# Kernel optimization log

Hardware: AMD Instinct MI355X
Metric: run time of the kernel (lower is better)

The kernel has to match this reference:

```python
import jax, jax.numpy as jnp
import numpy as np

B, S, D = 8, 2048, 256
H = 2
DK = D // H
DH = 1024  # conv hidden
K = 9
PAD = (K - 1) // 2
EPS = 1e-5


def _layernorm(x, g, b):
    mu = jnp.mean(x, axis=-1, keepdims=True)
    var = jnp.mean(jnp.square(x - mu), axis=-1, keepdims=True)
    return (x - mu) * jax.lax.rsqrt(var + EPS) * g + b


def setup_inputs() -> dict:
    key = jax.random.key(0)
    ks = jax.random.split(key, 12)
    sc = 0.02
    batch = jax.random.normal(ks[0], (B, S, D), dtype=jnp.float32)
    # padding mask: True = past end of sequence
    lengths = jax.random.randint(ks[1], (B,), S // 2, S + 1)
    mask = jnp.arange(S)[None, :] >= lengths[:, None]
    return {
        "batch": batch,
        "mask": mask,
        "wq": jax.random.normal(ks[2], (D, D), jnp.float32) * sc,
        "bq": jnp.zeros((D,), jnp.float32),
        "wk": jax.random.normal(ks[3], (D, D), jnp.float32) * sc,
        "bk": jnp.zeros((D,), jnp.float32),
        "wv": jax.random.normal(ks[4], (D, D), jnp.float32) * sc,
        "bv": jnp.zeros((D,), jnp.float32),
        "wo": jax.random.normal(ks[5], (D, D), jnp.float32) * sc,
        "bo": jnp.zeros((D,), jnp.float32),
        "ln1_g": jnp.ones((D,), jnp.float32),
        "ln1_b": jnp.zeros((D,), jnp.float32),
        "conv1_w": jax.random.normal(ks[6], (DH, D, K), jnp.float32) * sc,
        "conv1_b": jnp.zeros((DH,), jnp.float32),
        "conv2_w": jax.random.normal(ks[7], (D, DH, 1), jnp.float32) * sc,
        "conv2_b": jnp.zeros((D,), jnp.float32),
        "ln2_g": jnp.ones((D,), jnp.float32),
        "ln2_b": jnp.zeros((D,), jnp.float32),
    }


def reference(batch, mask, wq, bq, wk, bk, wv, bv, wo, bo, ln1_g, ln1_b,
              conv1_w, conv1_b, conv2_w, conv2_b, ln2_g, ln2_b):
    b, s, d = batch.shape
    # --- multi-head self-attention ---
    q = (batch @ wq.T + bq).reshape(b, s, H, DK)
    k = (batch @ wk.T + bk).reshape(b, s, H, DK)
    v = (batch @ wv.T + bv).reshape(b, s, H, DK)
    scores = jnp.einsum('bqhd,bkhd->bhqk', q, k) / np.sqrt(d).astype(np.float32)
    scores = jnp.where(mask[:, None, None, :], -jnp.inf, scores)
    attn = jax.nn.softmax(scores, axis=-1)
    ctx = jnp.einsum('bhqk,bkhd->bqhd', attn, v).reshape(b, s, d)
    seq = _layernorm(batch + ctx @ wo.T + bo, ln1_g, ln1_b)
    seq = jnp.where(mask[..., None], 0.0, seq)
    # --- conv FFN ---
    h = jax.lax.conv_general_dilated(
        seq.transpose(0, 2, 1), conv1_w, window_strides=(1,),
        padding=[(PAD, PAD)], dimension_numbers=('NCH', 'OIH', 'NCH'))
    h = jax.nn.relu(h + conv1_b[None, :, None])
    out = jnp.einsum('bhs,oh->bos', h, conv2_w[:, :, 0]) + conv2_b[None, :, None]
    seq = _layernorm(seq + out.transpose(0, 2, 1), ln2_g, ln2_b)
    return jnp.where(mask[..., None], 0.0, seq)
```

## Files before the change

kernel.cpp:

```cpp
#include <hip/hip_runtime.h>

typedef unsigned char  u8;
typedef unsigned short u16;
typedef unsigned int   u32;
typedef __attribute__((ext_vector_type(4))) float f32x4;
typedef __attribute__((ext_vector_type(8))) __bf16 bf16x8;
typedef __attribute__((ext_vector_type(4))) u32  u32x4;
typedef __attribute__((ext_vector_type(2))) u32  u32x2;

__device__ __forceinline__ float bf2f(u16 h){ u32 u = ((u32)h)<<16; return __builtin_bit_cast(float, u); }
__device__ __forceinline__ u16  f2bf(float f){
  u32 u = __builtin_bit_cast(u32, f);
  u32 r = u + 0x7FFFu + ((u>>16)&1u);
  return (u16)(r>>16);
}

typedef const __attribute__((address_space(1))) u32 gas_u32;
typedef __attribute__((address_space(3))) u32 las_u32;
__device__ __forceinline__ void gll16(const void* g, void* l){
  __builtin_amdgcn_global_load_lds((gas_u32*)g, (las_u32*)l, 16, 0, 0);
}

__device__ __forceinline__ f32x4 mfma16(bf16x8 a, bf16x8 b, f32x4 c){
  return __builtin_amdgcn_mfma_f32_16x16x32_bf16(a, b, c, 0, 0, 0);
}

__device__ __forceinline__ bf16x8 ldsr8(const u16* p){
  u32x4 v = *(const u32x4*)p;
  return __builtin_bit_cast(bf16x8, v);
}

__device__ __forceinline__ void xcd_remap(int &m_idx, int &n_idx){
  const int Mt = gridDim.x;
  const int fid = blockIdx.x + Mt*blockIdx.y;
  const int xcd = fid & 7, k = fid >> 3;
  const int mpx = Mt >> 3;
  m_idx = xcd*mpx + (k % mpx);
  n_idx = k / mpx;
}

__global__ __launch_bounds__(256)
void prep_big(const float* __restrict__ batch,
              const float* __restrict__ wq, const float* __restrict__ wk,
              const float* __restrict__ wv, const float* __restrict__ wo,
              const float* __restrict__ w2, const float* __restrict__ w1,
              u16* __restrict__ batchc, u16* __restrict__ wqc, u16* __restrict__ w1r)
{
  const int bid = blockIdx.x, tid = threadIdx.x;
  if (bid < 4096){
    const int i = bid*1024 + tid*4;
    f32x4 v = *(const f32x4*)&batch[i];
    u32x2 o;
    o[0] = (u32)f2bf(v[0]) | ((u32)f2bf(v[1])<<16);
    o[1] = (u32)f2bf(v[2]) | ((u32)f2bf(v[3])<<16);
    *(u32x2*)&batchc[i] = o;
  } else if (bid < 4608){
    const int i = (bid-4096)*1024 + tid*4;
    const float* s; int off;
    if      (i < 65536)  { s = wq; off = i; }
    else if (i < 131072) { s = wk; off = i - 65536; }
    else if (i < 196608) { s = wv; off = i - 131072; }
    else if (i < 262144) { s = wo; off = i - 196608; }
    else                 { s = w2; off = i - 262144; }
    f32x4 v = *(const f32x4*)&s[off];
    u32x2 o;
    o[0] = (u32)f2bf(v[0]) | ((u32)f2bf(v[1])<<16);
    o[1] = (u32)f2bf(v[2]) | ((u32)f2bf(v[3])<<16);
    *(u32x2*)&wqc[i] = o;
  } else {
    const int idx = (bid-4608)*256 + tid;
    const int c = idx / 2304;
    const int t = idx - c*2304;
    const int i = t / 9;
    const int kk = t - i*9;
    w1r[c*2304 + kk*256 + i] = f2bf(w1[idx]);
  }
}

__global__ __launch_bounds__(256)
void prep_small(const float* p0,const float* p1,const float* p2,const float* p3,
                const float* p4,const float* p5,const float* p6,const float* p7,
                const float* p8,const float* p9,
                u16* __restrict__ params, const void* __restrict__ mraw,
                u16* __restrict__ cmask, u32* __restrict__ lengths)
{
  const int bid = blockIdx.x, tid = threadIdx.x;
  if (bid == 0){
    const float* ps[10] = {p0,p1,p2,p3,p4,p5,p6,p7,p8,p9};
    const int  off[10] = {0,256,512,768,1024,1280,1536,1792,2048,3072};
    const int  len[10] = {256,256,256,256,256,256,256,256,1024,256};
    for (int a=0;a<10;++a)
      for (int i=tid;i<len[a];i+=256)
        params[off[a]+i] = f2bf(ps[a][i]);
  } else {
    const u8*  pb8  = (const u8*)mraw;
    const u16* pb16 = (const u16*)mraw;
    const u32* pb32 = (const u32*)mraw;
    __shared__ int bad8, bad16, nz8, nz16;
    __shared__ int slen[8];
    if (tid==0){ bad8=0; bad16=0; nz8=0; nz16=0; }
    if (tid<8) slen[tid] = 2048;
    __syncthreads();
    for (int i=tid;i<16384;i+=256){
      u8 v = pb8[i]; int row = i & 2047;
      if (v>1) atomicOr(&bad8,1);
      if (v){ atomicOr(&nz8,1); if (row<1024) atomicOr(&bad8,1); }
      if (row>0 && pb8[i-1]==1 && v==0) atomicOr(&bad8,1);
    }
    for (int i=tid;i<8192;i+=256){
      u16 v = pb16[i]; int row = i & 2047;
      if (!(v==0 || v==0x3F80)) atomicOr(&bad16,1);
      if (v){ atomicOr(&nz16,1); if (row<1024) atomicOr(&bad16,1); }
      if (row>0 && pb16[i-1]==0x3F80 && v==0) atomicOr(&bad16,1);
    }
    __syncthreads();
    const int mode = (!bad8 && nz8) ? 1 : ((!bad16 && nz16) ? 2 : 0);
    for (int i=tid;i<16384;i+=256){
      u16 m;
      if (mode==1)      m = pb8[i]  ? 1 : 0;
      else if (mode==2) m = pb16[i] ? 1 : 0;
      else              m = pb32[i] ? 1 : 0;
      cmask[i] = m;
      if (m) atomicMin(&slen[i>>11], i&2047);
    }
    __syncthreads();
    if (tid<8) lengths[tid] = (u32)slen[tid];
  }
}

__global__ __launch_bounds__(256)
void zero_halo(u16* __restrict__ seq1p)
{
  const int idx = blockIdx.x*256 + threadIdx.x;
  const int b = idx>>11, t = idx&2047;
  const int r = t>>8, c = t&255;
  const int row = (r<4) ? r : (2052 + r - 4);
  seq1p[((size_t)b*2056 + row)*256 + c] = 0;
}

__global__ __launch_bounds__(256)
void gemm_qkv(const u16* __restrict__ A, const u16* __restrict__ W,
              const u16* __restrict__ bias, u16* __restrict__ qbase,
              const u16* __restrict__ cmask)
{
  __shared__ __align__(16) u16 aL[2][4096];
  __shared__ __align__(16) u16 bL[2][4096];
  const int tid = threadIdx.x, lane = tid&63, w = tid>>6;
  const int wm = w>>1, wn = w&1, lr = lane&15, lg = lane>>4;
  int mi, ni; xcd_remap(mi, ni);
  const int m0 = mi*128, n0 = ni*128;
  if (cmask[m0] != 0) return;

  f32x4 acc[4][4];
#pragma unroll
  for (int i=0;i<4;++i)
#pragma unroll
    for (int j=0;j<4;++j) acc[i][j] = f32x4{0.f,0.f,0.f,0.f};

  auto stage = [&](int buf, int kk){
#pragma unroll
    for (int i=0;i<2;++i){
      const int chunk = w*2+i;
      const int boff  = chunk*1024 + lane*16;
      const int r = boff>>6;
      const int cb = (boff&63) ^ (((r>>1)&3)<<4);
      const int c = cb>>1;
      gll16(&A[(size_t)(m0+r)*256 + kk*32 + c], &aL[buf][chunk*512]);
      gll16(&W[(size_t)(n0+r)*256 + kk*32 + c], &bL[buf][chunk*512]);
    }
  };

  stage(0,0);
  __syncthreads();
  for (int kk=0; kk<8; ++kk){
    if (kk+1<8) stage((kk+1)&1, kk+1);
    const u16* ab = aL[kk&1];
    const u16* bb = bL[kk&1];
    bf16x8 af[4], bv[4];
#pragma unroll
    for (int m=0;m<4;++m){
      const int ra = wm*64+m*16+lr;
      af[m] = ldsr8(&ab[(ra*64 + ((lg*16) ^ (((ra>>1)&3)<<4)))>>1]);
    }
#pragma unroll
    for (int n=0;n<4;++n){
      const int rb = wn*64+n*16+lr;
      bv[n] = ldsr8(&bb[(rb*64 + ((lg*16) ^ (((rb>>1)&3)<<4)))>>1]);
    }
#pragma unroll
    for (int m=0;m<4;++m)
#pragma unroll
      for (int n=0;n<4;++n)
        acc[m][n] = mfma16(af[m], bv[n], acc[m][n]);
    __syncthreads();
  }
#pragma unroll
  for (int m=0;m<4;++m)
#pragma unroll
    for (int n=0;n<4;++n)
#pragma unroll
      for (int r=0;r<4;++r){
        const int row = m0 + wm*64 + m*16 + lg*4 + r;
        const int col = n0 + wn*64 + n*16 + lr;
        const int which = col>>8, ch = col&255;
        float v = acc[m][n][r] + bf2f(bias[col]);
        qbase[(size_t)which*4194304 + (size_t)row*256 + ch] = f2bf(v);
      }
}

__global__ __launch_bounds__(256, 4)
void conv1_gemm(const u16* __restrict__ Ap, const u16* __restrict__ W1r,
                const u16* __restrict__ b1, u16* __restrict__ Hout,
                const u16* __restrict__ cmask)
{
  __shared__ __align__(16) u16 aL[2][4096];
  __shared__ __align__(16) u16 bL[2][4096];
  const int tid = threadIdx.x, lane = tid&63, w = tid>>6;
  const int wm = w>>1, wn = w&1, lr = lane&15, lg = lane>>4;
  int mi, ni; xcd_remap(mi, ni);
  const int m0 = mi*128, n0 = ni*128;
  if (cmask[m0] != 0) return;
  const int b = m0>>11, s0 = m0&2047;
  const size_t abase = ((size_t)b*2056 + s0)*256;

  f32x4 acc[4][4];
#pragma unroll
  for (int i=0;i<4;++i)
#pragma unroll
    for (int j=0;j<4;++j) acc[i][j] = f32x4{0.f,0.f,0.f,0.f};

  auto stage = [&](int buf, int kk){
    const int tap = kk>>3, ch0 = (kk&7)*32;
#pragma unroll
    for (int i=0;i<2;++i){
      const int chunk = w*2+i;
      const int boff  = chunk*1024 + lane*16;
      const int r = boff>>6;
      const int cb = (boff&63) ^ (((r>>1)&3)<<4);
      const int c = cb>>1;
      gll16(&Ap[abase + (size_t)(tap + r)*256 + ch0 + c], &aL[buf][chunk*512]);
      gll16(&W1r[(size_t)(n0+r)*2304 + kk*32 + c], &bL[buf][chunk*512]);
    }
  };

  stage(0,0);
  __syncthreads();
  for (int kk=0; kk<72; ++kk){
    if (kk+1<72) stage((kk+1)&1, kk+1);
    const u16* ab = aL[kk&1];
    const u16* bb = bL[kk&1];
    bf16x8 af[4], bv[4];
#pragma unroll
    for (int m=0;m<4;++m){
      const int ra = wm*64+m*16+lr;
      af[m] = ldsr8(&ab[(ra*64 + ((lg*16) ^ (((ra>>1)&3)<<4)))>>1]);
    }
#pragma unroll
    for (int n=0;n<4;++n){
      const int rb = wn*64+n*16+lr;
      bv[n] = ldsr8(&bb[(rb*64 + ((lg*16) ^ (((rb>>1)&3)<<4)))>>1]);
    }
#pragma unroll
    for (int m=0;m<4;++m)
#pragma unroll
      for (int n=0;n<4;++n)
        acc[m][n] = mfma16(af[m], bv[n], acc[m][n]);
    __syncthreads();
  }
#pragma unroll
  for (int m=0;m<4;++m)
#pragma unroll
    for (int n=0;n<4;++n)
#pragma unroll
      for (int r=0;r<4;++r){
        const int row = m0 + wm*64 + m*16 + lg*4 + r;
        const int col = n0 + wn*64 + n*16 + lr;
        float v = acc[m][n][r] + bf2f(b1[col]);
        v = v>0.f ? v : 0.f;
        Hout[(size_t)row*1024 + col] = f2bf(v);
      }
}

__global__ __launch_bounds__(512)
void outproj_ln(const u16* __restrict__ Ctx, const u16* __restrict__ woc,
                const u16* __restrict__ bo, const u16* __restrict__ batchc,
                const u16* __restrict__ g1, const u16* __restrict__ be1,
                const u16* __restrict__ cmask, u16* __restrict__ seq1p)
{
  __shared__ __align__(16) u16 aL[2][2048];
  __shared__ __align__(16) u16 bL[2][8192];
  __shared__ float red[2][32][4][2];
  const int tid = threadIdx.x, lane = tid&63, w = tid>>6;
  const int wm = w>>2, wn = w&3, lr = lane&15, lg = lane>>4;
  int mi, ni; xcd_remap(mi, ni); (void)ni;
  const int m0 = mi*64;
  if (cmask[m0] != 0){
    for (int i=tid;i<64*128;i+=512){
      const int rr = i>>7, cc = (i&127)*2;
      const int row = m0 + rr;
      const size_t prow = (size_t)row + (row>>11)*8 + 4;
      *(u32*)&seq1p[prow*256 + cc] = 0u;
    }
    return;
  }

  f32x4 acc[2][4];
#pragma unroll
  for (int i=0;i<2;++i)
#pragma unroll
    for (int j=0;j<4;++j) acc[i][j] = f32x4{0.f,0.f,0.f,0.f};

  auto stage = [&](int buf, int kk){
    if (w < 4){
      const int boff = w*1024 + lane*16;
      const int r = boff>>6;
      const int cb = (boff&63) ^ (((r>>1)&3)<<4);
      gll16(&Ctx[(size_t)(m0+r)*256 + kk*32 + (cb>>1)], &aL[buf][w*512]);
    }
#pragma unroll
    for (int i=0;i<2;++i){
      const int chunk = w*2+i;
      const int boff = chunk*1024 + lane*16;
      const int r = boff>>6;
      const int cb = (boff&63) ^ (((r>>1)&3)<<4);
      gll16(&woc[(size_t)r*256 + kk*32 + (cb>>1)], &bL[buf][chunk*512]);
    }
  };

  stage(0,0);
  __syncthreads();
  for (int kk=0; kk<8; ++kk){
    if (kk+1<8) stage((kk+1)&1, kk+1);
    const u16* ab = aL[kk&1];
    const u16* bb = bL[kk&1];
    bf16x8 af[2], bv[4];
#pragma unroll
    for (int m=0;m<2;++m){
      const int ra = wm*32+m*16+lr;
      af[m] = ldsr8(&ab[(ra*64 + ((lg*16) ^ (((ra>>1)&3)<<4)))>>1]);
    }
#pragma unroll
    for (int n=0;n<4;++n){
      const int rb = wn*64+n*16+lr;
      bv[n] = ldsr8(&bb[(rb*64 + ((lg*16) ^ (((rb>>1)&3)<<4)))>>1]);
    }
#pragma unroll
    for (int m=0;m<2;++m)
#pragma unroll
      for (int n=0;n<4;++n)
        acc[m][n] = mfma16(af[m], bv[n], acc[m][n]);
    __syncthreads();
  }
#pragma unroll
  for (int m=0;m<2;++m)
#pragma unroll
    for (int r=0;r<4;++r){
      float s = 0.f, qq = 0.f;
#pragma unroll
      for (int n=0;n<4;++n){
        const int col = wn*64 + n*16 + lr;
        const int row = m0 + wm*32 + m*16 + lg*4 + r;
        float val = acc[m][n][r] + bf2f(bo[col]) + bf2f(batchc[(size_t)row*256 + col]);
        acc[m][n][r] = val;
        s += val; qq += val*val;
      }
#pragma unroll
      for (int x=1;x<16;x<<=1){ s += __shfl_xor(s, x); qq += __shfl_xor(qq, x); }
      if (lr == 0){
        const int lrow = m*16 + lg*4 + r;
        red[wm][lrow][wn][0] = s;
        red[wm][lrow][wn][1] = qq;
      }
    }
  __syncthreads();
#pragma unroll
  for (int m=0;m<2;++m)
#pragma unroll
    for (int r=0;r<4;++r){
      const int lrow = m*16 + lg*4 + r;
      const float S = red[wm][lrow][0][0]+red[wm][lrow][1][0]+red[wm][lrow][2][0]+red[wm][lrow][3][0];
      const float Q = red[wm][lrow][0][1]+red[wm][lrow][1][1]+red[wm][lrow][2][1]+red[wm][lrow][3][1];
      const float mu = S*(1.f/256.f);
      const float rs = rsqrtf(Q*(1.f/256.f) - mu*mu + 1e-5f);
      const int row = m0 + wm*32 + lrow;
      const int msk = cmask[row];
      const size_t prow = (size_t)row + (row>>11)*8 + 4;
#pragma unroll
      for (int n=0;n<4;++n){
        const int col = wn*64 + n*16 + lr;
        float y = (acc[m][n][r]-mu)*rs*bf2f(g1[col]) + bf2f(be1[col]);
        seq1p[prow*256 + col] = msk ? (u16)0 : f2bf(y);
      }
    }
}

__global__ __launch_bounds__(512)
void conv2_ln(const u16* __restrict__ Hh, const u16* __restrict__ w2c,
              const u16* __restrict__ b2, const u16* __restrict__ seq1p,
              const u16* __restrict__ g2, const u16* __restrict__ be2,
              const u16* __restrict__ cmask, float* __restrict__ out)
{
  __shared__ __align__(16) u16 aL[2][2048];
  __shared__ __align__(16) u16 bL[2][8192];
  __shared__ float red[2][32][4][2];
  const int tid = threadIdx.x, lane = tid&63, w = tid>>6;
  const int wm = w>>2, wn = w&3, lr = lane&15, lg = lane>>4;
  int mi, ni; xcd_remap(mi, ni); (void)ni;
  const int m0 = mi*64;
  if (cmask[m0] != 0) return;

  f32x4 acc[2][4];
#pragma unroll
  for (int i=0;i<2;++i)
#pragma unroll
    for (int j=0;j<4;++j) acc[i][j] = f32x4{0.f,0.f,0.f,0.f};

  auto stage = [&](int buf, int kk){
    if (w < 4){
      const int boff = w*1024 + lane*16;
      const int r = boff>>6;
      const int cb = (boff&63) ^ (((r>>1)&3)<<4);
      gll16(&Hh[(size_t)(m0+r)*1024 + kk*32 + (cb>>1)], &aL[buf][w*512]);
    }
#pragma unroll
    for (int i=0;i<2;++i){
      const int chunk = w*2+i;
      const int boff = chunk*1024 + lane*16;
      const int r = boff>>6;
      const int cb = (boff&63) ^ (((r>>1)&3)<<4);
      gll16(&w2c[(size_t)r*1024 + kk*32 + (cb>>1)], &bL[buf][chunk*512]);
    }
  };

  stage(0,0);
  __syncthreads();
  for (int kk=0; kk<32; ++kk){
    if (kk+1<32) stage((kk+1)&1, kk+1);
    const u16* ab = aL[kk&1];
    const u16* bb = bL[kk&1];
    bf16x8 af[2], bv[4];
#pragma unroll
    for (int m=0;m<2;++m){
      const int ra = wm*32+m*16+lr;
      af[m] = ldsr8(&ab[(ra*64 + ((lg*16) ^ (((ra>>1)&3)<<4)))>>1]);
    }
#pragma unroll
    for (int n=0;n<4;++n){
      const int rb = wn*64+n*16+lr;
      bv[n] = ldsr8(&bb[(rb*64 + ((lg*16) ^ (((rb>>1)&3)<<4)))>>1]);
    }
#pragma unroll
    for (int m=0;m<2;++m)
#pragma unroll
      for (int n=0;n<4;++n)
        acc[m][n] = mfma16(af[m], bv[n], acc[m][n]);
    __syncthreads();
  }
#pragma unroll
  for (int m=0;m<2;++m)
#pragma unroll
    for (int r=0;r<4;++r){
      float s = 0.f, qq = 0.f;
#pragma unroll
      for (int n=0;n<4;++n){
        const int col = wn*64 + n*16 + lr;
        const int row = m0 + wm*32 + m*16 + lg*4 + r;
        const size_t ri = ((size_t)row + (row>>11)*8 + 4)*256 + col;
        float val = acc[m][n][r] + bf2f(b2[col]) + bf2f(seq1p[ri]);
        acc[m][n][r] = val;
        s += val; qq += val*val;
      }
#pragma unroll
      for (int x=1;x<16;x<<=1){ s += __shfl_xor(s, x); qq += __shfl_xor(qq, x); }
      if (lr == 0){
        const int lrow = m*16 + lg*4 + r;
        red[wm][lrow][wn][0] = s;
        red[wm][lrow][wn][1] = qq;
      }
    }
  __syncthreads();
#pragma unroll
  for (int m=0;m<2;++m)
#pragma unroll
    for (int r=0;r<4;++r){
      const int lrow = m*16 + lg*4 + r;
      const float S = red[wm][lrow][0][0]+red[wm][lrow][1][0]+red[wm][lrow][2][0]+red[wm][lrow][3][0];
      const float Q = red[wm][lrow][0][1]+red[wm][lrow][1][1]+red[wm][lrow][2][1]+red[wm][lrow][3][1];
      const float mu = S*(1.f/256.f);
      const float rs = rsqrtf(Q*(1.f/256.f) - mu*mu + 1e-5f);
      const int row = m0 + wm*32 + lrow;
      const int msk = cmask[row];
#pragma unroll
      for (int n=0;n<4;++n){
        const int col = wn*64 + n*16 + lr;
        float y = (acc[m][n][r]-mu)*rs*bf2f(g2[col]) + bf2f(be2[col]);
        out[(size_t)row*256 + col] = msk ? 0.f : y;
      }
    }
}

__global__ __launch_bounds__(256)
void vtrans(const u16* __restrict__ V, u16* __restrict__ VT)
{
  __shared__ u16 t[64][72];
  const int tid = threadIdx.x;
  const int s0 = blockIdx.x*64;
  const int d0 = blockIdx.y*64;
#pragma unroll
  for (int i=0;i<2;++i){
    const int chunk = tid + i*256;
    const int sr = chunk>>3, c8 = (chunk&7)*8;
    u32x4 raw = *(const u32x4*)&V[(size_t)(s0+sr)*256 + d0 + c8];
#pragma unroll
    for (int j=0;j<4;++j){
      t[sr][c8+2*j]   = (u16)(raw[j]&0xffffu);
      t[sr][c8+2*j+1] = (u16)(raw[j]>>16);
    }
  }
  __syncthreads();
  const int b = s0>>11;
#pragma unroll
  for (int i=0;i<2;++i){
    const int chunk = tid + i*256;
    const int dr = chunk>>3, s8 = (chunk&7)*8;
    const int dg = d0 + dr;
    const int hh = dg>>7, dh = dg&127;
    u32x4 o;
#pragma unroll
    for (int j=0;j<4;++j)
      o[j] = (u32)t[s8+2*j][dr] | ((u32)t[s8+2*j+1][dr]<<16);
    *(u32x4*)&VT[((size_t)((b*2+hh)*128 + dh))*2048 + (s0&2047) + s8] = o;
  }
}

__global__ __launch_bounds__(512)
void attn_fwd(const u16* __restrict__ Q, const u16* __restrict__ Kb,
              const u16* __restrict__ VT, const u32* __restrict__ lengths,
              u16* __restrict__ ctx)
{
  __shared__ __align__(16) u16 kls[2][64*128];
  __shared__ __align__(16) u16 vtls[2][128*64];
  __shared__ __align__(16) u16 pls[8][16*64];
  const int tid = threadIdx.x, lane = tid&63, w = tid>>6;
  const int fid = blockIdx.x;
  const int pair = fid & 15;
  const int qt = fid >> 4;
  const int b  = pair >> 1;
  const int hh = pair & 1;
  const int q0 = qt*128;
  const int L  = (int)lengths[b];
  if (q0 >= L) return;
  const int nkt = (L + 63) >> 6;
  const int lr = lane&15, lg = lane>>4;
  u16* pw = pls[w];

  bf16x8 qf[4];
#pragma unroll
  for (int d=0;d<4;++d)
    qf[d] = *(const bf16x8*)&Q[((size_t)(b*2048+q0+w*16+lr))*256 + hh*128 + d*32 + lg*8];

  f32x4 oacc[8];
  float mrun[4], lrun[4];
#pragma unroll
  for (int n=0;n<8;++n) oacc[n] = f32x4{0.f,0.f,0.f,0.f};
#pragma unroll
  for (int r=0;r<4;++r){ mrun[r] = -1e30f; lrun[r] = 0.f; }

  const size_t kbase = (size_t)(b*2048)*256 + hh*128;
  const size_t vbase = (size_t)((b*2+hh)*128)*2048;

  auto stage = [&](int buf, int kt){
    const int kv0 = kt*64;
#pragma unroll
    for (int i=0;i<2;++i){
      const int chunk = w*2+i;
      const int boff = chunk*1024 + lane*16;
      const int r = boff>>8;
      const int cb = (boff&255) ^ ((r&7)<<4);
      gll16(&Kb[kbase + (size_t)(kv0+r)*256 + (cb>>1)], &kls[buf][chunk*512]);
    }
#pragma unroll
    for (int i=0;i<2;++i){
      const int chunk = w*2+i;
      const int boff = chunk*1024 + lane*16;
      const int r = boff>>7;
      const int cb = (boff&127) ^ ((r&7)<<4);
      gll16(&VT[vbase + (size_t)r*2048 + kv0 + (cb>>1)], &vtls[buf][chunk*512]);
    }
  };

  stage(0, 0);
  __syncthreads();

  for (int kt=0; kt<nkt; ++kt){
    const int kv0 = kt*64;
    const int buf = kt&1;
    if (kt+1 < nkt) stage(buf^1, kt+1);
    f32x4 sacc[4];
#pragma unroll
    for (int n=0;n<4;++n) sacc[n] = f32x4{0.f,0.f,0.f,0.f};
    __builtin_amdgcn_s_setprio(1);
#pragma unroll
    for (int dk=0;dk<4;++dk){
      bf16x8 bk[4];
#pragma unroll
      for (int n=0;n<4;++n){
        const int rb = n*16+lr;
        bk[n] = ldsr8(&kls[buf][(rb*256 + ((dk*64+lg*16) ^ ((rb&7)<<4)))>>1]);
      }
#pragma unroll
      for (int n=0;n<4;++n)
        sacc[n] = mfma16(qf[dk], bk[n], sacc[n]);
    }
    __builtin_amdgcn_s_setprio(0);
#pragma unroll
    for (int n=0;n<4;++n){
      const float madd = (kv0 + n*16 + lr < L) ? 0.f : -1e30f;
#pragma unroll
      for (int r=0;r<4;++r)
        sacc[n][r] = sacc[n][r]*0.0625f + madd;
    }
#pragma unroll
    for (int r=0;r<4;++r){
      float rm = sacc[0][r];
#pragma unroll
      for (int n=1;n<4;++n) rm = fmaxf(rm, sacc[n][r]);
#pragma unroll
      for (int x=1;x<16;x<<=1) rm = fmaxf(rm, __shfl_xor(rm, x));
      const float mnew = fmaxf(mrun[r], rm);
      const float alpha = __expf(mrun[r] - mnew);
      float rsum = 0.f;
#pragma unroll
      for (int n=0;n<4;++n){
        float p = __expf(sacc[n][r] - mnew);
        sacc[n][r] = p;
        rsum += p;
      }
#pragma unroll
      for (int x=1;x<16;x<<=1) rsum += __shfl_xor(rsum, x);
      lrun[r] = alpha*lrun[r] + rsum;
      mrun[r] = mnew;
#pragma unroll
      for (int n=0;n<8;++n) oacc[n][r] *= alpha;
    }
#pragma unroll
    for (int n=0;n<4;++n)
#pragma unroll
      for (int r=0;r<4;++r){
        const int row = lg*4 + r;
        pw[(row*128 + (((n*16+lr)*2) ^ ((row&7)<<4)))>>1] = f2bf(sacc[n][r]);
      }
    __builtin_amdgcn_s_setprio(1);
#pragma unroll
    for (int ks=0;ks<2;++ks){
      bf16x8 pa = ldsr8(&pw[(lr*128 + ((ks*64+lg*16) ^ ((lr&7)<<4)))>>1]);
#pragma unroll
      for (int n=0;n<8;++n){
        const int rv = n*16+lr;
        bf16x8 bvv = ldsr8(&vtls[buf][(rv*128 + ((ks*64+lg*16) ^ ((rv&7)<<4)))>>1]);
        oacc[n] = mfma16(pa, bvv, oacc[n]);
      }
    }
    __builtin_amdgcn_s_setprio(0);
    __syncthreads();
  }
#pragma unroll
  for (int r=0;r<4;++r){
    const float inv = lrun[r] > 0.f ? 1.f/lrun[r] : 0.f;
    const int row = q0 + w*16 + lg*4 + r;
#pragma unroll
    for (int n=0;n<8;++n){
      const int col = hh*128 + n*16 + lr;
      ctx[((size_t)(b*2048+row))*256 + col] = f2bf(oacc[n][r]*inv);
    }
  }
}

extern "C" void kernel_launch(void* const* d_in, const int* in_sizes, int n_in,
                              void* d_out, int out_size, void* d_ws, size_t ws_size,
                              hipStream_t stream)
{
  (void)in_sizes; (void)n_in; (void)out_size; (void)ws_size;
  const float* batch=(const float*)d_in[0];  const void* mraw = d_in[1];
  const float* wq=(const float*)d_in[2];  const float* bq=(const float*)d_in[3];
  const float* wk=(const float*)d_in[4];  const float* bk=(const float*)d_in[5];
  const float* wv=(const float*)d_in[6];  const float* bvv=(const float*)d_in[7];
  const float* wo=(const float*)d_in[8];  const float* bo=(const float*)d_in[9];
  const float* g1=(const float*)d_in[10]; const float* be1=(const float*)d_in[11];
  const float* w1=(const float*)d_in[12]; const float* b1=(const float*)d_in[13];
  const float* w2=(const float*)d_in[14]; const float* b2=(const float*)d_in[15];
  const float* g2=(const float*)d_in[16]; const float* be2=(const float*)d_in[17];

  char* ws = (char*)d_ws;
  const size_t M = 1024u*1024u;
  u16*   batchc = (u16*)(ws);
  u16*   q      = (u16*)(ws + 8*M);
  u16*   kbuf   = (u16*)(ws + 16*M);
  u16*   v      = (u16*)(ws + 24*M);
  u16*   ctx    = (u16*)(ws + 32*M);
  u16*   VT     = (u16*)(ws + 40*M);
  u16*   seq1p  = (u16*)(ws + 40*M);
  u16*   h      = (u16*)(ws);
  u16*   wqc    = (u16*)(ws + 49*M);
  u16*   woc    = wqc + 196608;
  u16*   w2c    = wqc + 262144;
  u16*   w1r    = (u16*)(ws + 50*M);
  u16*   params = w1r + 2359296;
  u16*   cmask  = params + 4096;
  u32*   lengths= (u32*)(cmask + 16384);

  dim3 blk(256,1,1);
  dim3 blk512(512,1,1);

  prep_big<<<dim3(13824,1,1), blk, 0, stream>>>(batch, wq, wk, wv, wo, w2, w1,
                                                batchc, wqc, w1r);
  prep_small<<<dim3(2,1,1), blk, 0, stream>>>(bq,bk,bvv,bo,g1,be1,g2,be2,b1,b2,
                                              params, mraw, cmask, lengths);

  gemm_qkv<<<dim3(128,6,1), blk, 0, stream>>>(batchc, wqc, params, q, cmask);

  vtrans<<<dim3(256,4,1), blk, 0, stream>>>(v, VT);

  attn_fwd<<<dim3(256,1,1), blk512, 0, stream>>>(q, kbuf, VT, lengths, ctx);

  zero_halo<<<dim3(64,1,1), blk, 0, stream>>>(seq1p);

  outproj_ln<<<dim3(256,1,1), blk512, 0, stream>>>(ctx, woc, params+768, batchc,
                                                   params+1024, params+1280, cmask, seq1p);

  conv1_gemm<<<dim3(128,8,1), blk, 0, stream>>>(seq1p, w1r, params+2048, h, cmask);

  conv2_ln<<<dim3(256,1,1), blk512, 0, stream>>>(h, w2c, params+3072, seq1p,
                                                 params+1536, params+1792, cmask,
                                                 (float*)d_out);
}
```

Before: 289.6 us.

## Fuse V transpose into QKV GEMM epilogue and drop vtrans kernel

The QKV GEMM epilogue now writes the V projection directly in transposed per-head layout, so the separate vtrans kernel and the intermediate V buffer are removed. This saves one launch and a full read and write of V. The transposed stores are strided scalar 16-bit writes, which may coalesce poorly. Separately, conv1_gemm replaces the XCD-aware block remap with a plain linear block-to-tile mapping.

Measured after the change: 305.1 us. 1.05x slower.

```diff
diff --git a/kernel.cpp b/kernel.cpp
--- a/kernel.cpp
+++ b/kernel.cpp
@@ -141,7 +141,7 @@
 __global__ __launch_bounds__(256)
 void gemm_qkv(const u16* __restrict__ A, const u16* __restrict__ W,
               const u16* __restrict__ bias, u16* __restrict__ qbase,
-              const u16* __restrict__ cmask)
+              u16* __restrict__ VT, const u16* __restrict__ cmask)
 {
   __shared__ __align__(16) u16 aL[2][4096];
   __shared__ __align__(16) u16 bL[2][4096];
@@ -194,18 +194,35 @@
         acc[m][n] = mfma16(af[m], bv[n], acc[m][n]);
     __syncthreads();
   }
-#pragma unroll
-  for (int m=0;m<4;++m)
-#pragma unroll
-    for (int n=0;n<4;++n)
-#pragma unroll
-      for (int r=0;r<4;++r){
-        const int row = m0 + wm*64 + m*16 + lg*4 + r;
-        const int col = n0 + wn*64 + n*16 + lr;
-        const int which = col>>8, ch = col&255;
-        float v = acc[m][n][r] + bf2f(bias[col]);
-        qbase[(size_t)which*4194304 + (size_t)row*256 + ch] = f2bf(v);
-      }
+  if (n0 < 512){
+#pragma unroll
+    for (int m=0;m<4;++m)
+#pragma unroll
+      for (int n=0;n<4;++n)
+#pragma unroll
+        for (int r=0;r<4;++r){
+          const int row = m0 + wm*64 + m*16 + lg*4 + r;
+          const int col = n0 + wn*64 + n*16 + lr;
+          const int which = col>>8, ch = col&255;
+          float v = acc[m][n][r] + bf2f(bias[col]);
+          qbase[(size_t)which*4194304 + (size_t)row*256 + ch] = f2bf(v);
+        }
+  } else {
+#pragma unroll
+    for (int m=0;m<4;++m)
+#pragma unroll
+      for (int n=0;n<4;++n)
+#pragma unroll
+        for (int r=0;r<4;++r){
+          const int row = m0 + wm*64 + m*16 + lg*4 + r;
+          const int col = n0 + wn*64 + n*16 + lr;
+          const int ch = col&255;
+          const int hh = ch>>7, dh = ch&127;
+          const int b = row>>11, s = row&2047;
+          float v = acc[m][n][r] + bf2f(bias[col]);
+          VT[((size_t)((b*2+hh)*128 + dh))*2048 + s] = f2bf(v);
+        }
+  }
 }
 
 __global__ __launch_bounds__(256, 4)
@@ -217,7 +234,8 @@
   __shared__ __align__(16) u16 bL[2][4096];
   const int tid = threadIdx.x, lane = tid&63, w = tid>>6;
   const int wm = w>>1, wn = w&1, lr = lane&15, lg = lane>>4;
-  int mi, ni; xcd_remap(mi, ni);
+  const int fid = blockIdx.x + gridDim.x*blockIdx.y;
+  const int mi = fid >> 3, ni = fid & 7;
   const int m0 = mi*128, n0 = ni*128;
   if (cmask[m0] != 0) return;
   const int b = m0>>11, s0 = m0&2047;
@@ -497,40 +515,6 @@
         out[(size_t)row*256 + col] = msk ? 0.f : y;
       }
     }
-}
-
-__global__ __launch_bounds__(256)
-void vtrans(const u16* __restrict__ V, u16* __restrict__ VT)
-{
-  __shared__ u16 t[64][72];
-  const int tid = threadIdx.x;
-  const int s0 = blockIdx.x*64;
-  const int d0 = blockIdx.y*64;
-#pragma unroll
-  for (int i=0;i<2;++i){
-    const int chunk = tid + i*256;
-    const int sr = chunk>>3, c8 = (chunk&7)*8;
-    u32x4 raw = *(const u32x4*)&V[(size_t)(s0+sr)*256 + d0 + c8];
-#pragma unroll
-    for (int j=0;j<4;++j){
-      t[sr][c8+2*j]   = (u16)(raw[j]&0xffffu);
-      t[sr][c8+2*j+1] = (u16)(raw[j]>>16);
-    }
-  }
-  __syncthreads();
-  const int b = s0>>11;
-#pragma unroll
-  for (int i=0;i<2;++i){
-    const int chunk = tid + i*256;
-    const int dr = chunk>>3, s8 = (chunk&7)*8;
-    const int dg = d0 + dr;
-    const int hh = dg>>7, dh = dg&127;
-    u32x4 o;
-#pragma unroll
-    for (int j=0;j<4;++j)
-      o[j] = (u32)t[s8+2*j][dr] | ((u32)t[s8+2*j+1][dr]<<16);
-    *(u32x4*)&VT[((size_t)((b*2+hh)*128 + dh))*2048 + (s0&2047) + s8] = o;
-  }
 }
 
 __global__ __launch_bounds__(512)
@@ -696,7 +680,6 @@
   u16*   batchc = (u16*)(ws);
   u16*   q      = (u16*)(ws + 8*M);
   u16*   kbuf   = (u16*)(ws + 16*M);
-  u16*   v      = (u16*)(ws + 24*M);
   u16*   ctx    = (u16*)(ws + 32*M);
   u16*   VT     = (u16*)(ws + 40*M);
   u16*   seq1p  = (u16*)(ws + 40*M);
@@ -717,9 +700,7 @@
   prep_small<<<dim3(2,1,1), blk, 0, stream>>>(bq,bk,bvv,bo,g1,be1,g2,be2,b1,b2,
                                               params, mraw, cmask, lengths);
 
-  gemm_qkv<<<dim3(128,6,1), blk, 0, stream>>>(batchc, wqc, params, q, cmask);
-
-  vtrans<<<dim3(256,4,1), blk, 0, stream>>>(v, VT);
+  gemm_qkv<<<dim3(128,6,1), blk, 0, stream>>>(batchc, wqc, params, q, VT, cmask);
 
   attn_fwd<<<dim3(256,1,1), blk512, 0, stream>>>(q, kbuf, VT, lengths, ctx);
 
```
